# Optimization experiments

Hardware: AMD Instinct MI355X
Metric: run time of the kernel (lower is better)

Reference implementation:

```python
import jax, jax.numpy as jnp
import numpy as np

GAMMA = 2.0
NUM_CLASSES = 33

def _cdist(x):
    # pairwise euclidean distance per batch: x [B,N,C] -> [B,N,N]
    sq = jnp.sum(x * x, axis=-1)                      # [B,N]
    d2 = sq[:, :, None] + sq[:, None, :] - 2.0 * jnp.einsum('bnc,bmc->bnm', x, x)
    d2 = jnp.maximum(d2, 0.0)
    d = jnp.sqrt(jnp.where(d2 > 0, d2, 1.0))          # safe sqrt (zero-distance -> 0, no nan grad)
    return jnp.where(d2 > 0, d, 0.0)


def setup_inputs() -> dict:
    key = jax.random.key(0)
    k1, k2, k3 = jax.random.split(key, 3)
    B, N, C = 2, 4096, NUM_CLASSES
    predictions = jax.random.normal(k1, (B, N, C), dtype=jnp.float32)
    targets = jax.random.randint(k2, (B, N), 0, C, dtype=jnp.int32)
    y_ohe = jax.nn.one_hot(targets, C, dtype=jnp.float32)
    pred_choice = jax.random.randint(k3, (B, N), 0, C, dtype=jnp.int32)
    return {"predictions": predictions, "y_ohe": y_ohe, "targets": targets, "pred_choice": pred_choice}


def reference(predictions, y_ohe, targets, pred_choice):
    B, N, C = predictions.shape
    # cross-entropy (mean over all B*N positions, no class weights)
    logp = jax.nn.log_softmax(predictions, axis=-1)                       # [B,N,C]
    logp_t = jnp.take_along_axis(logp, targets[..., None].astype(jnp.int32), axis=-1)[..., 0]
    ce_loss = -jnp.mean(logp_t)                                           # scalar

    # distance-map KL term
    dis_map = _cdist(y_ohe)                                               # [B,N,N]
    dis_map = jnp.where(dis_map > 1.0, 0.9, dis_map)
    dis_map = jnp.where(dis_map < 1.0, 0.05, dis_map)
    pred_prob = jax.nn.softmax(predictions, axis=-1)
    pred_map = _cdist(pred_prob)                                          # [B,N,N]
    # torch F.kl_div(input, target) with default 'mean': mean(target*(log(target)-input))
    dis_map_loss = jnp.mean(dis_map * (jnp.log(dis_map) - pred_map))

    # focal weighting of the (scalar) CE loss
    pn = jnp.take_along_axis(jnp.exp(logp), targets[..., None].astype(jnp.int32), axis=-1)[..., 0]
    pn = pn.reshape(-1)                                                   # [B*N]
    loss = jnp.mean((1.0 - pn) ** GAMMA * ce_loss)

    # dice loss: per-class loop collapses exactly to a global match count
    eps = 1.0
    matches = jnp.sum((targets.reshape(-1) == pred_choice.reshape(-1)).astype(jnp.float32))
    total = targets.size
    dice = 1.0 - 2.0 * ((matches + eps) / (2.0 * total + eps))

    return loss + dice + dis_map_loss
```

## Files before the change

### kernel.cpp

```cpp
#include <hip/hip_runtime.h>
#include <math.h>

#define BB 2
#define NN 4096
#define CC 33
#define RP 40
#define TILE 64
#define NTILES (NN / TILE)
#define NPB 1056
#define ROWBLK ((BB * NN) / 8)
#define PAIRBLK (BB * NPB)
#define NSLOT 64
#define SLOTSTR 32

typedef __attribute__((ext_vector_type(8))) short frag_ab;
typedef __attribute__((ext_vector_type(4))) float f32x4;

__device__ __forceinline__ float fast_sqrt(float x) {
    return __builtin_amdgcn_sqrtf(x);
}
__device__ __forceinline__ unsigned short f2bf(float x) {
    unsigned u = __float_as_uint(x);
    return (unsigned short)((u + 0x7FFFu + ((u >> 16) & 1u)) >> 16);
}
__device__ __forceinline__ float bf2f(unsigned short b) {
    return __uint_as_float(((unsigned)b) << 16);
}

__global__ __launch_bounds__(512) void row_kernel(
    const float* __restrict__ pred, const int* __restrict__ targets,
    const int* __restrict__ pred_choice, unsigned short* __restrict__ p16,
    float* __restrict__ sqn, float2* __restrict__ part_row,
    int* __restrict__ part_match, float* __restrict__ slotf,
    unsigned* __restrict__ subcnt, unsigned* __restrict__ master)
{
    __shared__ float2 lds_cf[8];
    __shared__ int lds_mt[8];

    if (blockIdx.x == 0) {
        for (int i = threadIdx.x; i < NSLOT * SLOTSTR; i += 512) {
            slotf[i] = 0.0f;
            subcnt[i] = 0u;
        }
        if (threadIdx.x == 0) *master = 0u;
    }

    int lane = threadIdx.x & 63;
    int wave = threadIdx.x >> 6;
    int row = blockIdx.x * 8 + wave;

    float v = (lane < CC) ? pred[(size_t)row * CC + lane] : -INFINITY;

    float m = v;
    #pragma unroll
    for (int off = 32; off; off >>= 1) m = fmaxf(m, __shfl_xor(m, off));

    float e = (lane < CC) ? __expf(v - m) : 0.0f;
    float s = e;
    #pragma unroll
    for (int off = 32; off; off >>= 1) s += __shfl_xor(s, off);

    float pv = e / s;

    unsigned short pb = f2bf(pv);
    if (lane < RP) p16[(size_t)row * RP + lane] = pb;

    float pf = bf2f(pb);
    float sq = pf * pf;
    #pragma unroll
    for (int off = 32; off; off >>= 1) sq += __shfl_xor(sq, off);

    int t = targets[row];
    float vt = __shfl(v, t);
    float pt = __shfl(pv, t);
    float logpt = (vt - m) - __logf(s);

    if (lane == 0) {
        sqn[row] = sq;
        float om = 1.0f - pt;
        lds_cf[wave] = make_float2(-logpt, om * om);
        lds_mt[wave] = (t == pred_choice[row]) ? 1 : 0;
    }
    __syncthreads();
    if (threadIdx.x == 0) {
        float ce = 0.0f, fo = 0.0f;
        int mt = 0;
        #pragma unroll
        for (int i = 0; i < 8; i++) {
            ce += lds_cf[i].x; fo += lds_cf[i].y; mt += lds_mt[i];
        }
        part_row[blockIdx.x] = make_float2(ce, fo);
        part_match[blockIdx.x] = mt;
    }
}

__global__ __launch_bounds__(256) void pair_kernel(
    const unsigned short* __restrict__ p16, const float* __restrict__ sqn,
    const float2* __restrict__ part_row, const int* __restrict__ part_match,
    float* __restrict__ slotf, unsigned* __restrict__ subcnt,
    unsigned* __restrict__ master, float* __restrict__ out)
{
    __shared__ __align__(16) unsigned short spi[TILE * RP];
    __shared__ __align__(16) unsigned short spj[2][TILE * RP];
    __shared__ float ssqi[TILE], ssqj[2][TILE];
    __shared__ float red[4];
    __shared__ int lastFlag;
    __shared__ double lds_ce[4], lds_fo[4], lds_pr[4];
    __shared__ int lds_mt[4];

    int bid = blockIdx.x;
    int b = bid / NPB;
    int t = bid % NPB;

    int ti = 0, rem = t;
    while (rem >= 32 - (ti >> 1)) { rem -= 32 - (ti >> 1); ++ti; }
    int tjA = ti + 2 * rem;
    bool hasB = (tjA + 1 < NTILES);
    bool diagA = (tjA == ti);

    int i0 = ti * TILE;
    int j0A = tjA * TILE;

    const float4* srci  = (const float4*)(p16 + ((size_t)b * NN + i0) * RP);
    const float4* srcjA = (const float4*)(p16 + ((size_t)b * NN + j0A) * RP);
    float4* di  = (float4*)spi;
    float4* djA = (float4*)spj[0];
    for (int k = threadIdx.x; k < TILE * (RP / 8); k += 256) {
        di[k]  = srci[k];
        djA[k] = srcjA[k];
    }
    if (hasB) {
        const float4* srcjB = srcjA + TILE * (RP / 8);
        float4* djB = (float4*)spj[1];
        for (int k = threadIdx.x; k < TILE * (RP / 8); k += 256)
            djB[k] = srcjB[k];
    }
    if (threadIdx.x < TILE)
        ssqi[threadIdx.x] = sqn[b * NN + i0 + threadIdx.x];
    else if (threadIdx.x < 2 * TILE)
        ssqj[0][threadIdx.x - TILE] = sqn[b * NN + j0A + (threadIdx.x - TILE)];
    else if (hasB && threadIdx.x < 3 * TILE)
        ssqj[1][threadIdx.x - 2 * TILE] = sqn[b * NN + j0A + TILE + (threadIdx.x - 2 * TILE)];
    __syncthreads();

    int l = threadIdx.x & 63;
    int w = threadIdx.x >> 6;
    int col = l & 15;
    int kc = l >> 4;

    frag_ab afr = *(const frag_ab*)&spi[(16 * w + col) * RP + kc * 8];

    float qi[4], c32a[4];
    #pragma unroll
    for (int r = 0; r < 4; r++) {
        int ir = 16 * w + kc * 4 + r;
        qi[r]   = ssqi[ir];
        c32a[r] = bf2f(spi[ir * RP + 32]);
    }
    int gi0 = i0 + 16 * w + kc * 4;

    float ssum = 0.0f;

    #pragma unroll
    for (int jt = 0; jt < 2; jt++) {
        if (jt == 1 && !hasB) break;
        const unsigned short* spjx = spj[jt];
        const float* ssqx = ssqj[jt];
        int j0 = j0A + jt * TILE;
        bool dg = (jt == 0) && diagA;

        #pragma unroll
        for (int n = 0; n < 4; n++) {
            frag_ab bfr = *(const frag_ab*)&spjx[(16 * n + col) * RP + kc * 8];
            f32x4 acc = {0.0f, 0.0f, 0.0f, 0.0f};
            acc = __builtin_amdgcn_mfma_f32_16x16x32_bf16(afr, bfr, acc, 0, 0, 0);

            float c32b = bf2f(spjx[(16 * n + col) * RP + 32]);
            float qj   = ssqx[16 * n + col];
            int   gj   = j0 + 16 * n + col;

            #pragma unroll
            for (int r = 0; r < 4; r++) {
                float g  = fmaf(c32a[r], c32b, acc[r]);
                float d2 = fmaf(-2.0f, g, qi[r] + qj);
                float d  = fast_sqrt(fmaxf(d2, 0.0f));
                ssum += (!dg || gj > gi0 + r) ? d : 0.0f;
            }
        }
    }

    #pragma unroll
    for (int off = 32; off; off >>= 1) ssum += __shfl_xor(ssum, off);
    if (l == 0) red[w] = ssum;
    __syncthreads();

    if (threadIdx.x == 0) {
        float blockSum = red[0] + red[1] + red[2] + red[3];
        int slot = (bid & (NSLOT - 1)) * SLOTSTR;
        __hip_atomic_fetch_add(&slotf[slot], blockSum,
                               __ATOMIC_RELAXED, __HIP_MEMORY_SCOPE_AGENT);
        asm volatile("s_waitcnt vmcnt(0)" ::: "memory");
        unsigned o = __hip_atomic_fetch_add(&subcnt[slot], 1u,
                                            __ATOMIC_RELAXED, __HIP_MEMORY_SCOPE_AGENT);
        int last = 0;
        if (o == (PAIRBLK / NSLOT) - 1) {
            unsigned o2 = __hip_atomic_fetch_add(master, 1u,
                                                 __ATOMIC_RELAXED, __HIP_MEMORY_SCOPE_AGENT);
            last = (o2 == NSLOT - 1);
        }
        lastFlag = last;
    }
    __syncthreads();
    if (!lastFlag) return;

    double ce = 0.0, fo = 0.0, pr = 0.0;
    int mt = 0;
    for (int i = threadIdx.x; i < ROWBLK; i += 256) {
        float2 v = part_row[i];
        ce += (double)v.x;
        fo += (double)v.y;
        mt += part_match[i];
    }
    for (int i = threadIdx.x; i < NSLOT; i += 256)
        pr += (double)__hip_atomic_load(&slotf[i * SLOTSTR],
                                        __ATOMIC_RELAXED, __HIP_MEMORY_SCOPE_AGENT);

    #pragma unroll
    for (int off = 32; off; off >>= 1) {
        ce += __shfl_xor(ce, off);
        fo += __shfl_xor(fo, off);
        pr += __shfl_xor(pr, off);
        mt += __shfl_xor(mt, off);
    }
    if (l == 0) { lds_ce[w] = ce; lds_fo[w] = fo; lds_pr[w] = pr; lds_mt[w] = mt; }
    __syncthreads();
    if (threadIdx.x == 0) {
        double tce = lds_ce[0] + lds_ce[1] + lds_ce[2] + lds_ce[3];
        double tfo = lds_fo[0] + lds_fo[1] + lds_fo[2] + lds_fo[3];
        double tpr = lds_pr[0] + lds_pr[1] + lds_pr[2] + lds_pr[3];
        int    tmt = lds_mt[0] + lds_mt[1] + lds_mt[2] + lds_mt[3];

        double BN = (double)(BB * NN);
        double loss = (tce / BN) * (tfo / BN);
        double dice = 1.0 - 2.0 * ((double)tmt + 1.0) / (2.0 * BN + 1.0);
        double S = 2.0 * tpr;
        double mean_pred = S / (BN * (double)NN);
        double dml = 0.05 * log(0.05) - 0.05 * mean_pred;
        out[0] = (float)(loss + dice + dml);
    }
}

extern "C" void kernel_launch(void* const* d_in, const int* in_sizes, int n_in,
                              void* d_out, int out_size, void* d_ws, size_t ws_size,
                              hipStream_t stream)
{
    const float* pred        = (const float*)d_in[0];
    const int*   targets     = (const int*)d_in[2];
    const int*   pred_choice = (const int*)d_in[3];

    char* ws = (char*)d_ws;
    size_t off = 0;
    unsigned short* p16 = (unsigned short*)ws;
    off += (size_t)BB * NN * RP * sizeof(unsigned short);
    float* sqn = (float*)(ws + off);
    off += (size_t)BB * NN * sizeof(float);
    off = (off + 127) & ~(size_t)127;
    float2* part_row = (float2*)(ws + off);
    off += (size_t)ROWBLK * sizeof(float2);
    int* part_match = (int*)(ws + off);
    off += (size_t)ROWBLK * sizeof(int);
    off = (off + 127) & ~(size_t)127;
    float* slotf = (float*)(ws + off);
    off += (size_t)NSLOT * SLOTSTR * sizeof(float);
    unsigned* subcnt = (unsigned*)(ws + off);
    off += (size_t)NSLOT * SLOTSTR * sizeof(unsigned);
    unsigned* master = (unsigned*)(ws + off);
    off += sizeof(unsigned);

    row_kernel<<<ROWBLK, 512, 0, stream>>>(pred, targets, pred_choice,
                                           p16, sqn, part_row, part_match,
                                           slotf, subcnt, master);
    pair_kernel<<<PAIRBLK, 256, 0, stream>>>(p16, sqn, part_row, part_match,
                                             slotf, subcnt, master, (float*)d_out);
}
```

Before: 21.89 us.

## Fuse row softmax into pair kernel, recomputing bf16 probabilities per tile

Drops the separate row kernel. Each pair block now loads raw fp32 logits for its i and j tiles, computes softmax, bf16 packing and squared norms in shared memory, then runs the MFMA distance pass. CE, focal and match terms are produced only by diagonal blocks and written to per-block partials. The slot-based atomic reduction is replaced by a single counter reset with a memset. This removes a kernel launch and the global round trip for p16 and sqn, but every block redoes softmax for up to 192 rows, and the scalar per-thread softmax plus the uncoalesced scatter into shared memory adds latency.

```diff
diff --git a/kernel.cpp b/kernel.cpp
--- a/kernel.cpp
+++ b/kernel.cpp
@@ -4,14 +4,12 @@
 #define BB 2
 #define NN 4096
 #define CC 33
-#define RP 40
 #define TILE 64
 #define NTILES (NN / TILE)
 #define NPB 1056
-#define ROWBLK ((BB * NN) / 8)
 #define PAIRBLK (BB * NPB)
-#define NSLOT 64
-#define SLOTSTR 32
+#define NDIAG (BB * NTILES)
+#define RPF 36
 
 typedef __attribute__((ext_vector_type(8))) short frag_ab;
 typedef __attribute__((ext_vector_type(4))) float f32x4;
@@ -19,90 +17,23 @@
 __device__ __forceinline__ float fast_sqrt(float x) {
     return __builtin_amdgcn_sqrtf(x);
 }
-__device__ __forceinline__ unsigned short f2bf(float x) {
+__device__ __forceinline__ unsigned f2bf(float x) {
     unsigned u = __float_as_uint(x);
-    return (unsigned short)((u + 0x7FFFu + ((u >> 16) & 1u)) >> 16);
-}
-__device__ __forceinline__ float bf2f(unsigned short b) {
-    return __uint_as_float(((unsigned)b) << 16);
-}
-
-__global__ __launch_bounds__(512) void row_kernel(
+    return (u + 0x7FFFu + ((u >> 16) & 1u)) >> 16;
+}
+__device__ __forceinline__ float bf2f(unsigned b) {
+    return __uint_as_float(b << 16);
+}
+
+__global__ __launch_bounds__(256) void fused_kernel(
     const float* __restrict__ pred, const int* __restrict__ targets,
-    const int* __restrict__ pred_choice, unsigned short* __restrict__ p16,
-    float* __restrict__ sqn, float2* __restrict__ part_row,
-    int* __restrict__ part_match, float* __restrict__ slotf,
-    unsigned* __restrict__ subcnt, unsigned* __restrict__ master)
-{
-    __shared__ float2 lds_cf[8];
-    __shared__ int lds_mt[8];
-
-    if (blockIdx.x == 0) {
-        for (int i = threadIdx.x; i < NSLOT * SLOTSTR; i += 512) {
-            slotf[i] = 0.0f;
-            subcnt[i] = 0u;
-        }
-        if (threadIdx.x == 0) *master = 0u;
-    }
-
-    int lane = threadIdx.x & 63;
-    int wave = threadIdx.x >> 6;
-    int row = blockIdx.x * 8 + wave;
-
-    float v = (lane < CC) ? pred[(size_t)row * CC + lane] : -INFINITY;
-
-    float m = v;
-    #pragma unroll
-    for (int off = 32; off; off >>= 1) m = fmaxf(m, __shfl_xor(m, off));
-
-    float e = (lane < CC) ? __expf(v - m) : 0.0f;
-    float s = e;
-    #pragma unroll
-    for (int off = 32; off; off >>= 1) s += __shfl_xor(s, off);
-
-    float pv = e / s;
-
-    unsigned short pb = f2bf(pv);
-    if (lane < RP) p16[(size_t)row * RP + lane] = pb;
-
-    float pf = bf2f(pb);
-    float sq = pf * pf;
-    #pragma unroll
-    for (int off = 32; off; off >>= 1) sq += __shfl_xor(sq, off);
-
-    int t = targets[row];
-    float vt = __shfl(v, t);
-    float pt = __shfl(pv, t);
-    float logpt = (vt - m) - __logf(s);
-
-    if (lane == 0) {
-        sqn[row] = sq;
-        float om = 1.0f - pt;
-        lds_cf[wave] = make_float2(-logpt, om * om);
-        lds_mt[wave] = (t == pred_choice[row]) ? 1 : 0;
-    }
-    __syncthreads();
-    if (threadIdx.x == 0) {
-        float ce = 0.0f, fo = 0.0f;
-        int mt = 0;
-        #pragma unroll
-        for (int i = 0; i < 8; i++) {
-            ce += lds_cf[i].x; fo += lds_cf[i].y; mt += lds_mt[i];
-        }
-        part_row[blockIdx.x] = make_float2(ce, fo);
-        part_match[blockIdx.x] = mt;
-    }
-}
-
-__global__ __launch_bounds__(256) void pair_kernel(
-    const unsigned short* __restrict__ p16, const float* __restrict__ sqn,
-    const float2* __restrict__ part_row, const int* __restrict__ part_match,
-    float* __restrict__ slotf, unsigned* __restrict__ subcnt,
+    const int* __restrict__ pred_choice,
+    float* __restrict__ part_pair, float* __restrict__ part_ce,
+    float* __restrict__ part_fo, int* __restrict__ part_mt,
     unsigned* __restrict__ master, float* __restrict__ out)
 {
-    __shared__ __align__(16) unsigned short spi[TILE * RP];
-    __shared__ __align__(16) unsigned short spj[2][TILE * RP];
-    __shared__ float ssqi[TILE], ssqj[2][TILE];
+    __shared__ __align__(16) float sraw[192 * RPF];
+    __shared__ float ssq[192];
     __shared__ float red[4];
     __shared__ int lastFlag;
     __shared__ double lds_ce[4], lds_fo[4], lds_pr[4];
@@ -110,81 +41,125 @@
 
     int bid = blockIdx.x;
     int b = bid / NPB;
-    int t = bid % NPB;
-
-    int ti = 0, rem = t;
+    int t0 = bid % NPB;
+
+    int ti = 0, rem = t0;
     while (rem >= 32 - (ti >> 1)) { rem -= 32 - (ti >> 1); ++ti; }
     int tjA = ti + 2 * rem;
     bool hasB = (tjA + 1 < NTILES);
     bool diagA = (tjA == ti);
-
-    int i0 = ti * TILE;
-    int j0A = tjA * TILE;
-
-    const float4* srci  = (const float4*)(p16 + ((size_t)b * NN + i0) * RP);
-    const float4* srcjA = (const float4*)(p16 + ((size_t)b * NN + j0A) * RP);
-    float4* di  = (float4*)spi;
-    float4* djA = (float4*)spj[0];
-    for (int k = threadIdx.x; k < TILE * (RP / 8); k += 256) {
-        di[k]  = srci[k];
-        djA[k] = srcjA[k];
-    }
-    if (hasB) {
-        const float4* srcjB = srcjA + TILE * (RP / 8);
-        float4* djB = (float4*)spj[1];
-        for (int k = threadIdx.x; k < TILE * (RP / 8); k += 256)
-            djB[k] = srcjB[k];
-    }
-    if (threadIdx.x < TILE)
-        ssqi[threadIdx.x] = sqn[b * NN + i0 + threadIdx.x];
-    else if (threadIdx.x < 2 * TILE)
-        ssqj[0][threadIdx.x - TILE] = sqn[b * NN + j0A + (threadIdx.x - TILE)];
-    else if (hasB && threadIdx.x < 3 * TILE)
-        ssqj[1][threadIdx.x - 2 * TILE] = sqn[b * NN + j0A + TILE + (threadIdx.x - 2 * TILE)];
-    __syncthreads();
-
-    int l = threadIdx.x & 63;
-    int w = threadIdx.x >> 6;
-    int col = l & 15;
-    int kc = l >> 4;
-
-    frag_ab afr = *(const frag_ab*)&spi[(16 * w + col) * RP + kc * 8];
-
+    int i0 = ti * TILE, j0A = tjA * TILE;
+    int jcnt = hasB ? 128 : 64;
+
+    {
+        const float4* srcI = (const float4*)(pred + ((size_t)b * NN + i0) * CC);
+        const float4* srcJ = (const float4*)(pred + ((size_t)b * NN + j0A) * CC);
+        int jf4 = (jcnt * CC) / 4;
+        int tot = 528 + jf4;
+        for (int k = threadIdx.x; k < tot; k += 256) {
+            int isJ = (k >= 528);
+            int kk = isJ ? k - 528 : k;
+            float4 val = isJ ? srcJ[kk] : srcI[kk];
+            int rowoff = isJ ? 64 : 0;
+            int flat = kk * 4;
+            float vv[4] = {val.x, val.y, val.z, val.w};
+            #pragma unroll
+            for (int e = 0; e < 4; e++) {
+                int f = flat + e;
+                int r = f / CC;
+                int c = f - r * CC;
+                sraw[(rowoff + r) * RPF + c] = vv[e];
+            }
+        }
+    }
+    __syncthreads();
+
+    float ce = 0.f, fo = 0.f; int mt = 0;
+    {
+        int t = threadIdx.x;
+        if (t < 64 + jcnt) {
+            int base = t * RPF;
+            float v[33];
+            #pragma unroll
+            for (int c = 0; c < 33; c++) v[c] = sraw[base + c];
+            float m = v[0];
+            #pragma unroll
+            for (int c = 1; c < 33; c++) m = fmaxf(m, v[c]);
+            float s = 0.f;
+            #pragma unroll
+            for (int c = 0; c < 33; c++) { v[c] = __expf(v[c] - m); s += v[c]; }
+            if (diagA && t < 64) {
+                int g = b * NN + i0 + t;
+                int tg = targets[g];
+                float vt = sraw[base + tg];
+                float logpt = (vt - m) - __logf(s);
+                ce = -logpt;
+                float pt = __expf(vt - m) / s;
+                float om = 1.f - pt;
+                fo = om * om;
+                mt = (tg == pred_choice[g]) ? 1 : 0;
+            }
+            float inv = 1.f / s;
+            unsigned d[17];
+            float q = 0.f;
+            #pragma unroll
+            for (int k = 0; k < 16; k++) {
+                unsigned lo = f2bf(v[2 * k] * inv);
+                unsigned hi = f2bf(v[2 * k + 1] * inv);
+                float fl = bf2f(lo), fh = bf2f(hi);
+                q += fl * fl + fh * fh;
+                d[k] = lo | (hi << 16);
+            }
+            {
+                unsigned lo = f2bf(v[32] * inv);
+                float fl = bf2f(lo);
+                q += fl * fl;
+                d[16] = lo;
+            }
+            unsigned* dd = (unsigned*)sraw + base;
+            #pragma unroll
+            for (int k = 0; k < 17; k++) dd[k] = d[k];
+            ssq[t] = q;
+        }
+    }
+    __syncthreads();
+
+    int l = threadIdx.x & 63, w = threadIdx.x >> 6;
+    int col = l & 15, kc = l >> 4;
+    const unsigned short* sus = (const unsigned short*)sraw;
+
+    frag_ab afr = *(const frag_ab*)&sus[(16 * w + col) * 72 + kc * 8];
     float qi[4], c32a[4];
     #pragma unroll
     for (int r = 0; r < 4; r++) {
         int ir = 16 * w + kc * 4 + r;
-        qi[r]   = ssqi[ir];
-        c32a[r] = bf2f(spi[ir * RP + 32]);
+        qi[r] = ssq[ir];
+        c32a[r] = bf2f(sus[ir * 72 + 32]);
     }
     int gi0 = i0 + 16 * w + kc * 4;
 
-    float ssum = 0.0f;
-
+    float ssum = 0.f;
     #pragma unroll
     for (int jt = 0; jt < 2; jt++) {
         if (jt == 1 && !hasB) break;
-        const unsigned short* spjx = spj[jt];
-        const float* ssqx = ssqj[jt];
-        int j0 = j0A + jt * TILE;
+        int rbase = 64 + jt * 64;
+        int j0 = (tjA + jt) * TILE;
         bool dg = (jt == 0) && diagA;
-
         #pragma unroll
         for (int n = 0; n < 4; n++) {
-            frag_ab bfr = *(const frag_ab*)&spjx[(16 * n + col) * RP + kc * 8];
-            f32x4 acc = {0.0f, 0.0f, 0.0f, 0.0f};
+            int jr = rbase + 16 * n + col;
+            frag_ab bfr = *(const frag_ab*)&sus[jr * 72 + kc * 8];
+            f32x4 acc = {0.f, 0.f, 0.f, 0.f};
             acc = __builtin_amdgcn_mfma_f32_16x16x32_bf16(afr, bfr, acc, 0, 0, 0);
-
-            float c32b = bf2f(spjx[(16 * n + col) * RP + 32]);
-            float qj   = ssqx[16 * n + col];
-            int   gj   = j0 + 16 * n + col;
-
+            float c32b = bf2f(sus[jr * 72 + 32]);
+            float qj = ssq[jr];
+            int gj = j0 + 16 * n + col;
             #pragma unroll
             for (int r = 0; r < 4; r++) {
                 float g  = fmaf(c32a[r], c32b, acc[r]);
-                float d2 = fmaf(-2.0f, g, qi[r] + qj);
-                float d  = fast_sqrt(fmaxf(d2, 0.0f));
-                ssum += (!dg || gj > gi0 + r) ? d : 0.0f;
+                float d2 = fmaf(-2.f, g, qi[r] + qj);
+                float dd = fast_sqrt(fmaxf(d2, 0.f));
+                ssum += (!dg || gj > gi0 + r) ? dd : 0.f;
             }
         }
     }
@@ -192,47 +167,54 @@
     #pragma unroll
     for (int off = 32; off; off >>= 1) ssum += __shfl_xor(ssum, off);
     if (l == 0) red[w] = ssum;
-    __syncthreads();
-
+    if (w == 0) {
+        #pragma unroll
+        for (int off = 32; off; off >>= 1) {
+            ce += __shfl_xor(ce, off);
+            fo += __shfl_xor(fo, off);
+            mt += __shfl_xor(mt, off);
+        }
+    }
+    __syncthreads();
     if (threadIdx.x == 0) {
         float blockSum = red[0] + red[1] + red[2] + red[3];
-        int slot = (bid & (NSLOT - 1)) * SLOTSTR;
-        __hip_atomic_fetch_add(&slotf[slot], blockSum,
-                               __ATOMIC_RELAXED, __HIP_MEMORY_SCOPE_AGENT);
+        __hip_atomic_store(&part_pair[bid], blockSum,
+                           __ATOMIC_RELAXED, __HIP_MEMORY_SCOPE_AGENT);
+        if (diagA) {
+            int did = b * NTILES + ti;
+            __hip_atomic_store(&part_ce[did], ce, __ATOMIC_RELAXED, __HIP_MEMORY_SCOPE_AGENT);
+            __hip_atomic_store(&part_fo[did], fo, __ATOMIC_RELAXED, __HIP_MEMORY_SCOPE_AGENT);
+            __hip_atomic_store(&part_mt[did], mt, __ATOMIC_RELAXED, __HIP_MEMORY_SCOPE_AGENT);
+        }
         asm volatile("s_waitcnt vmcnt(0)" ::: "memory");
-        unsigned o = __hip_atomic_fetch_add(&subcnt[slot], 1u,
+        unsigned o = __hip_atomic_fetch_add(master, 1u,
                                             __ATOMIC_RELAXED, __HIP_MEMORY_SCOPE_AGENT);
-        int last = 0;
-        if (o == (PAIRBLK / NSLOT) - 1) {
-            unsigned o2 = __hip_atomic_fetch_add(master, 1u,
-                                                 __ATOMIC_RELAXED, __HIP_MEMORY_SCOPE_AGENT);
-            last = (o2 == NSLOT - 1);
-        }
-        lastFlag = last;
+        lastFlag = (o == PAIRBLK - 1);
     }
     __syncthreads();
     if (!lastFlag) return;
 
-    double ce = 0.0, fo = 0.0, pr = 0.0;
-    int mt = 0;
-    for (int i = threadIdx.x; i < ROWBLK; i += 256) {
-        float2 v = part_row[i];
-        ce += (double)v.x;
-        fo += (double)v.y;
-        mt += part_match[i];
-    }
-    for (int i = threadIdx.x; i < NSLOT; i += 256)
-        pr += (double)__hip_atomic_load(&slotf[i * SLOTSTR],
-                                        __ATOMIC_RELAXED, __HIP_MEMORY_SCOPE_AGENT);
-
+    double dce = 0.0, dfo = 0.0, dpr = 0.0;
+    int dmt = 0;
+    for (int i = threadIdx.x; i < PAIRBLK; i += 256)
+        dpr += (double)__hip_atomic_load(&part_pair[i],
+                                         __ATOMIC_RELAXED, __HIP_MEMORY_SCOPE_AGENT);
+    for (int i = threadIdx.x; i < NDIAG; i += 256) {
+        dce += (double)__hip_atomic_load(&part_ce[i],
+                                         __ATOMIC_RELAXED, __HIP_MEMORY_SCOPE_AGENT);
+        dfo += (double)__hip_atomic_load(&part_fo[i],
+                                         __ATOMIC_RELAXED, __HIP_MEMORY_SCOPE_AGENT);
+        dmt += __hip_atomic_load(&part_mt[i],
+                                 __ATOMIC_RELAXED, __HIP_MEMORY_SCOPE_AGENT);
+    }
     #pragma unroll
     for (int off = 32; off; off >>= 1) {
-        ce += __shfl_xor(ce, off);
-        fo += __shfl_xor(fo, off);
-        pr += __shfl_xor(pr, off);
-        mt += __shfl_xor(mt, off);
-    }
-    if (l == 0) { lds_ce[w] = ce; lds_fo[w] = fo; lds_pr[w] = pr; lds_mt[w] = mt; }
+        dce += __shfl_xor(dce, off);
+        dfo += __shfl_xor(dfo, off);
+        dpr += __shfl_xor(dpr, off);
+        dmt += __shfl_xor(dmt, off);
+    }
+    if (l == 0) { lds_ce[w] = dce; lds_fo[w] = dfo; lds_pr[w] = dpr; lds_mt[w] = dmt; }
     __syncthreads();
     if (threadIdx.x == 0) {
         double tce = lds_ce[0] + lds_ce[1] + lds_ce[2] + lds_ce[3];
@@ -260,26 +242,20 @@
 
     char* ws = (char*)d_ws;
     size_t off = 0;
-    unsigned short* p16 = (unsigned short*)ws;
-    off += (size_t)BB * NN * RP * sizeof(unsigned short);
-    float* sqn = (float*)(ws + off);
-    off += (size_t)BB * NN * sizeof(float);
+    float* part_pair = (float*)ws;
+    off += (size_t)PAIRBLK * sizeof(float);
+    float* part_ce = (float*)(ws + off);
+    off += (size_t)NDIAG * sizeof(float);
+    float* part_fo = (float*)(ws + off);
+    off += (size_t)NDIAG * sizeof(float);
+    int* part_mt = (int*)(ws + off);
+    off += (size_t)NDIAG * sizeof(int);
     off = (off + 127) & ~(size_t)127;
-    float2* part_row = (float2*)(ws + off);
-    off += (size_t)ROWBLK * sizeof(float2);
-    int* part_match = (int*)(ws + off);
-    off += (size_t)ROWBLK * sizeof(int);
-    off = (off + 127) & ~(size_t)127;
-    float* slotf = (float*)(ws + off);
-    off += (size_t)NSLOT * SLOTSTR * sizeof(float);
-    unsigned* subcnt = (unsigned*)(ws + off);
-    off += (size_t)NSLOT * SLOTSTR * sizeof(unsigned);
     unsigned* master = (unsigned*)(ws + off);
     off += sizeof(unsigned);
 
-    row_kernel<<<ROWBLK, 512, 0, stream>>>(pred, targets, pred_choice,
-                                           p16, sqn, part_row, part_match,
-                                           slotf, subcnt, master);
-    pair_kernel<<<PAIRBLK, 256, 0, stream>>>(p16, sqn, part_row, part_match,
-                                             slotf, subcnt, master, (float*)d_out);
-}
+    hipMemsetAsync(master, 0, sizeof(unsigned), stream);
+    fused_kernel<<<PAIRBLK, 256, 0, stream>>>(pred, targets, pred_choice,
+                                              part_pair, part_ce, part_fo,
+                                              part_mt, master, (float*)d_out);
+}
```

Result: slower. 42.80 us (+95.5%).

## Load pair-kernel fragments directly from global memory and compute tile index in closed form

Applied to the files above, without the earlier changes.

The pair kernel no longer stages the i/j tile data and squared norms in shared memory behind a barrier. Each lane now reads its MFMA fragments, the extra 33rd-column element and the norms straight from global memory, relying on L1/L2 caching. The triangular tile index is found with a sqrt-based closed-form estimate plus correction loops instead of a linear search loop. This removes LDS traffic and a __syncthreads, at the cost of redundant, less coalesced global loads.

```diff
diff --git a/kernel.cpp b/kernel.cpp
--- a/kernel.cpp
+++ b/kernel.cpp
@@ -100,9 +100,6 @@
     float* __restrict__ slotf, unsigned* __restrict__ subcnt,
     unsigned* __restrict__ master, float* __restrict__ out)
 {
-    __shared__ __align__(16) unsigned short spi[TILE * RP];
-    __shared__ __align__(16) unsigned short spj[2][TILE * RP];
-    __shared__ float ssqi[TILE], ssqj[2][TILE];
     __shared__ float red[4];
     __shared__ int lastFlag;
     __shared__ double lds_ce[4], lds_fo[4], lds_pr[4];
@@ -112,50 +109,38 @@
     int b = bid / NPB;
     int t = bid % NPB;
 
-    int ti = 0, rem = t;
-    while (rem >= 32 - (ti >> 1)) { rem -= 32 - (ti >> 1); ++ti; }
-    int tjA = ti + 2 * rem;
+    int p = (int)(32.5f - fast_sqrt(fmaxf(1056.25f - (float)t, 0.0f)));
+    if (p < 0) p = 0;
+    if (p > 31) p = 31;
+    while (p > 0 && p * (65 - p) > t) --p;
+    while (p < 31 && (p + 1) * (64 - p) <= t) ++p;
+    int rem = t - p * (65 - p);
+    int c0 = 32 - p;
+    int ti = 2 * p + (rem >= c0);
+    int u = (rem >= c0) ? rem - c0 : rem;
+    int tjA = ti + 2 * u;
     bool hasB = (tjA + 1 < NTILES);
     bool diagA = (tjA == ti);
 
-    int i0 = ti * TILE;
-    int j0A = tjA * TILE;
-
-    const float4* srci  = (const float4*)(p16 + ((size_t)b * NN + i0) * RP);
-    const float4* srcjA = (const float4*)(p16 + ((size_t)b * NN + j0A) * RP);
-    float4* di  = (float4*)spi;
-    float4* djA = (float4*)spj[0];
-    for (int k = threadIdx.x; k < TILE * (RP / 8); k += 256) {
-        di[k]  = srci[k];
-        djA[k] = srcjA[k];
-    }
-    if (hasB) {
-        const float4* srcjB = srcjA + TILE * (RP / 8);
-        float4* djB = (float4*)spj[1];
-        for (int k = threadIdx.x; k < TILE * (RP / 8); k += 256)
-            djB[k] = srcjB[k];
-    }
-    if (threadIdx.x < TILE)
-        ssqi[threadIdx.x] = sqn[b * NN + i0 + threadIdx.x];
-    else if (threadIdx.x < 2 * TILE)
-        ssqj[0][threadIdx.x - TILE] = sqn[b * NN + j0A + (threadIdx.x - TILE)];
-    else if (hasB && threadIdx.x < 3 * TILE)
-        ssqj[1][threadIdx.x - 2 * TILE] = sqn[b * NN + j0A + TILE + (threadIdx.x - 2 * TILE)];
-    __syncthreads();
+    int i0 = ti * TILE, j0A = tjA * TILE;
 
     int l = threadIdx.x & 63;
     int w = threadIdx.x >> 6;
     int col = l & 15;
     int kc = l >> 4;
 
-    frag_ab afr = *(const frag_ab*)&spi[(16 * w + col) * RP + kc * 8];
+    const unsigned short* pb16 = p16 + (size_t)b * NN * RP;
+    const float* sqb = sqn + (size_t)b * NN;
+
+    int arow = i0 + 16 * w + col;
+    frag_ab afr = *(const frag_ab*)&pb16[(size_t)arow * RP + kc * 8];
 
     float qi[4], c32a[4];
     #pragma unroll
     for (int r = 0; r < 4; r++) {
-        int ir = 16 * w + kc * 4 + r;
-        qi[r]   = ssqi[ir];
-        c32a[r] = bf2f(spi[ir * RP + 32]);
+        int ir = i0 + 16 * w + kc * 4 + r;
+        qi[r]   = sqb[ir];
+        c32a[r] = bf2f(pb16[(size_t)ir * RP + 32]);
     }
     int gi0 = i0 + 16 * w + kc * 4;
 
@@ -164,20 +149,19 @@
     #pragma unroll
     for (int jt = 0; jt < 2; jt++) {
         if (jt == 1 && !hasB) break;
-        const unsigned short* spjx = spj[jt];
-        const float* ssqx = ssqj[jt];
         int j0 = j0A + jt * TILE;
         bool dg = (jt == 0) && diagA;
 
         #pragma unroll
         for (int n = 0; n < 4; n++) {
-            frag_ab bfr = *(const frag_ab*)&spjx[(16 * n + col) * RP + kc * 8];
+            int jrow = j0 + 16 * n + col;
+            frag_ab bfr = *(const frag_ab*)&pb16[(size_t)jrow * RP + kc * 8];
             f32x4 acc = {0.0f, 0.0f, 0.0f, 0.0f};
             acc = __builtin_amdgcn_mfma_f32_16x16x32_bf16(afr, bfr, acc, 0, 0, 0);
 
-            float c32b = bf2f(spjx[(16 * n + col) * RP + 32]);
-            float qj   = ssqx[16 * n + col];
-            int   gj   = j0 + 16 * n + col;
+            float c32b = bf2f(pb16[(size_t)jrow * RP + 32]);
+            float qj   = sqb[jrow];
+            int   gj   = jrow;
 
             #pragma unroll
             for (int r = 0; r < 4; r++) {
```

Result: slower. 23.18 us (+5.9%).

## Restructure row softmax to 8 lanes per row and closed-form pair tile index

Applied to the files above, without the earlier changes.

The row kernel now stages 32 rows of predictions into shared memory with coalesced float4 loads. Each row is then handled by 8 lanes that hold 4 classes each, with 3-step shuffle reductions and packed bf16 stores, instead of one 64-lane wave per row. This cuts the per-row reduction depth and the number of blocks launched. The pair kernel replaces its serial loop for mapping a block to a triangular tile pair with a sqrt-based closed form plus a small correction step. The part_row and part_match partial counts now come from 256 blocks instead of 1024, which the second kernel's final reduction must agree with.

```diff
diff --git a/kernel.cpp b/kernel.cpp
--- a/kernel.cpp
+++ b/kernel.cpp
@@ -8,7 +8,7 @@
 #define TILE 64
 #define NTILES (NN / TILE)
 #define NPB 1056
-#define ROWBLK ((BB * NN) / 8)
+#define ROWBLK 256
 #define PAIRBLK (BB * NPB)
 #define NSLOT 64
 #define SLOTSTR 32
@@ -19,78 +19,123 @@
 __device__ __forceinline__ float fast_sqrt(float x) {
     return __builtin_amdgcn_sqrtf(x);
 }
-__device__ __forceinline__ unsigned short f2bf(float x) {
+__device__ __forceinline__ unsigned f2bf(float x) {
     unsigned u = __float_as_uint(x);
-    return (unsigned short)((u + 0x7FFFu + ((u >> 16) & 1u)) >> 16);
-}
-__device__ __forceinline__ float bf2f(unsigned short b) {
-    return __uint_as_float(((unsigned)b) << 16);
-}
-
-__global__ __launch_bounds__(512) void row_kernel(
+    return (u + 0x7FFFu + ((u >> 16) & 1u)) >> 16;
+}
+__device__ __forceinline__ float bf2f(unsigned b) {
+    return __uint_as_float(b << 16);
+}
+
+__global__ __launch_bounds__(256) void row_kernel(
     const float* __restrict__ pred, const int* __restrict__ targets,
     const int* __restrict__ pred_choice, unsigned short* __restrict__ p16,
     float* __restrict__ sqn, float2* __restrict__ part_row,
     int* __restrict__ part_match, float* __restrict__ slotf,
     unsigned* __restrict__ subcnt, unsigned* __restrict__ master)
 {
-    __shared__ float2 lds_cf[8];
-    __shared__ int lds_mt[8];
+    __shared__ __align__(16) float sraw[32 * CC];
+    __shared__ float2 lds_cf[4];
+    __shared__ int lds_mt[4];
 
     if (blockIdx.x == 0) {
-        for (int i = threadIdx.x; i < NSLOT * SLOTSTR; i += 512) {
+        for (int i = threadIdx.x; i < NSLOT * SLOTSTR; i += 256) {
             slotf[i] = 0.0f;
             subcnt[i] = 0u;
         }
         if (threadIdx.x == 0) *master = 0u;
     }
 
-    int lane = threadIdx.x & 63;
-    int wave = threadIdx.x >> 6;
-    int row = blockIdx.x * 8 + wave;
-
-    float v = (lane < CC) ? pred[(size_t)row * CC + lane] : -INFINITY;
-
-    float m = v;
-    #pragma unroll
-    for (int off = 32; off; off >>= 1) m = fmaxf(m, __shfl_xor(m, off));
-
-    float e = (lane < CC) ? __expf(v - m) : 0.0f;
-    float s = e;
-    #pragma unroll
-    for (int off = 32; off; off >>= 1) s += __shfl_xor(s, off);
-
-    float pv = e / s;
-
-    unsigned short pb = f2bf(pv);
-    if (lane < RP) p16[(size_t)row * RP + lane] = pb;
-
-    float pf = bf2f(pb);
-    float sq = pf * pf;
-    #pragma unroll
-    for (int off = 32; off; off >>= 1) sq += __shfl_xor(sq, off);
-
-    int t = targets[row];
-    float vt = __shfl(v, t);
-    float pt = __shfl(pv, t);
-    float logpt = (vt - m) - __logf(s);
-
-    if (lane == 0) {
+    {
+        const float4* src = (const float4*)(pred + (size_t)blockIdx.x * 32 * CC);
+        float4* dst = (float4*)sraw;
+        for (int k = threadIdx.x; k < 264; k += 256) dst[k] = src[k];
+    }
+    __syncthreads();
+
+    int l = threadIdx.x & 63;
+    int w = threadIdx.x >> 6;
+    int r = l >> 3;
+    int c = l & 7;
+    int rloc = w * 8 + r;
+    int row = blockIdx.x * 32 + rloc;
+
+    float v[4];
+    #pragma unroll
+    for (int k = 0; k < 4; k++) v[k] = sraw[rloc * CC + 4 * c + k];
+    float v32 = sraw[rloc * CC + 32];
+
+    float m = fmaxf(fmaxf(v[0], v[1]), fmaxf(v[2], v[3]));
+    if (c == 0) m = fmaxf(m, v32);
+    m = fmaxf(m, __shfl_xor(m, 1));
+    m = fmaxf(m, __shfl_xor(m, 2));
+    m = fmaxf(m, __shfl_xor(m, 4));
+
+    float e[4];
+    float s = 0.0f;
+    #pragma unroll
+    for (int k = 0; k < 4; k++) { e[k] = __expf(v[k] - m); s += e[k]; }
+    float e32 = __expf(v32 - m);
+    if (c == 0) s += e32;
+    s += __shfl_xor(s, 1);
+    s += __shfl_xor(s, 2);
+    s += __shfl_xor(s, 4);
+    float inv = 1.0f / s;
+
+    unsigned pb[4];
+    float sq = 0.0f;
+    #pragma unroll
+    for (int k = 0; k < 4; k++) {
+        pb[k] = f2bf(e[k] * inv);
+        float pf = bf2f(pb[k]);
+        sq += pf * pf;
+    }
+    unsigned c32u = f2bf(e32 * inv);
+    float c32 = bf2f(c32u);
+    if (c == 0) sq += c32 * c32;
+    sq += __shfl_xor(sq, 1);
+    sq += __shfl_xor(sq, 2);
+    sq += __shfl_xor(sq, 4);
+
+    {
+        uint2 st = make_uint2(pb[0] | (pb[1] << 16), pb[2] | (pb[3] << 16));
+        *(uint2*)&p16[(size_t)row * RP + 4 * c] = st;
+    }
+    if (c == 0) {
+        uint4 st = make_uint4(c32u, 0u, 0u, 0u);
+        *(uint4*)&p16[(size_t)row * RP + 32] = st;
         sqn[row] = sq;
+    }
+
+    int tg = targets[row];
+    float cand = 0.0f;
+    if (tg < 32) {
+        int cc = tg >> 2, kk = tg & 3;
+        if (cc == c) cand = e[kk];
+    } else if (c == 0) cand = e32;
+    cand += __shfl_xor(cand, 1);
+    cand += __shfl_xor(cand, 2);
+    cand += __shfl_xor(cand, 4);
+
+    float ce = 0.0f, fo = 0.0f; int mt = 0;
+    if (c == 0) {
+        float pt = cand * inv;
+        ce = -__logf(pt);
         float om = 1.0f - pt;
-        lds_cf[wave] = make_float2(-logpt, om * om);
-        lds_mt[wave] = (t == pred_choice[row]) ? 1 : 0;
-    }
+        fo = om * om;
+        mt = (tg == pred_choice[row]) ? 1 : 0;
+    }
+    ce += __shfl_xor(ce, 8);  ce += __shfl_xor(ce, 16);  ce += __shfl_xor(ce, 32);
+    fo += __shfl_xor(fo, 8);  fo += __shfl_xor(fo, 16);  fo += __shfl_xor(fo, 32);
+    mt += __shfl_xor(mt, 8);  mt += __shfl_xor(mt, 16);  mt += __shfl_xor(mt, 32);
+
+    if (l == 0) { lds_cf[w] = make_float2(ce, fo); lds_mt[w] = mt; }
     __syncthreads();
     if (threadIdx.x == 0) {
-        float ce = 0.0f, fo = 0.0f;
-        int mt = 0;
-        #pragma unroll
-        for (int i = 0; i < 8; i++) {
-            ce += lds_cf[i].x; fo += lds_cf[i].y; mt += lds_mt[i];
-        }
-        part_row[blockIdx.x] = make_float2(ce, fo);
-        part_match[blockIdx.x] = mt;
+        float2 a = lds_cf[0], b2 = lds_cf[1], c2 = lds_cf[2], d = lds_cf[3];
+        part_row[blockIdx.x] = make_float2(a.x + b2.x + c2.x + d.x,
+                                           a.y + b2.y + c2.y + d.y);
+        part_match[blockIdx.x] = lds_mt[0] + lds_mt[1] + lds_mt[2] + lds_mt[3];
     }
 }
 
@@ -112,14 +157,20 @@
     int b = bid / NPB;
     int t = bid % NPB;
 
-    int ti = 0, rem = t;
-    while (rem >= 32 - (ti >> 1)) { rem -= 32 - (ti >> 1); ++ti; }
-    int tjA = ti + 2 * rem;
+    int p = (int)(32.5f - fast_sqrt(fmaxf(1056.25f - (float)t, 0.0f)));
+    if (p < 0) p = 0;
+    if (p > 31) p = 31;
+    while (p > 0 && p * (65 - p) > t) --p;
+    while (p < 31 && (p + 1) * (64 - p) <= t) ++p;
+    int rem = t - p * (65 - p);
+    int c0 = 32 - p;
+    int ti = 2 * p + (rem >= c0);
+    int u = (rem >= c0) ? rem - c0 : rem;
+    int tjA = ti + 2 * u;
     bool hasB = (tjA + 1 < NTILES);
     bool diagA = (tjA == ti);
 
-    int i0 = ti * TILE;
-    int j0A = tjA * TILE;
+    int i0 = ti * TILE, j0A = tjA * TILE;
 
     const float4* srci  = (const float4*)(p16 + ((size_t)b * NN + i0) * RP);
     const float4* srcjA = (const float4*)(p16 + ((size_t)b * NN + j0A) * RP);
@@ -277,7 +328,7 @@
     unsigned* master = (unsigned*)(ws + off);
     off += sizeof(unsigned);
 
-    row_kernel<<<ROWBLK, 512, 0, stream>>>(pred, targets, pred_choice,
+    row_kernel<<<ROWBLK, 256, 0, stream>>>(pred, targets, pred_choice,
                                            p16, sqn, part_row, part_match,
                                            slotf, subcnt, master);
     pair_kernel<<<PAIRBLK, 256, 0, stream>>>(p16, sqn, part_row, part_match,
```

New measurement: 21.21 us. 3.1% less time.
